# Optimization experiments

Hardware: AMD Instinct MI355X
Metric: run time of the kernel (lower is better)

The kernel has to match this reference:

```python
import jax, jax.numpy as jnp
import numpy as np

LEAKY = 0.2  # tf.nn.leaky_relu default alpha
E_SZ = [64, 64, 16]
F_SZ = [128, 128, 8]
N_MAPS, C, H, W = 64, 1, 32, 32
B = 8192


def _leaky(x):
    return jnp.where(x >= 0, x, LEAKY * x)


def func_theta(x, theta, sz, in_sz):
    # x: [B, in_sz]; theta: [B, total]; per-sample MLP with weights sliced from theta
    y = x
    offset = 0
    n = len(sz)
    for i, out_sz in enumerate(sz):
        w_sz = in_sz * out_sz
        Wm = theta[:, offset:offset + w_sz].reshape(-1, in_sz, out_sz)
        offset += w_sz
        b = theta[:, offset:offset + out_sz]
        offset += out_sz
        y = jnp.einsum('bi,bio->bo', y, Wm) + b
        if i < n - 1:
            y = _leaky(y)
        in_sz = out_sz
    return y


def setup_inputs() -> dict:
    key = jax.random.key(0)
    ks = jax.random.split(key, 16)

    def g(k, shape, scale):
        return (jax.random.normal(k, shape, dtype=jnp.float32) * scale)

    inp = {
        'indices': jax.random.randint(ks[0], (B,), 0, N_MAPS, dtype=jnp.int32),
        'states': jax.random.normal(ks[1], (B, 4), dtype=jnp.float32),
        'maps': jax.random.normal(ks[2], (N_MAPS, C, H, W), dtype=jnp.float32),
        'fc1_w': g(ks[3], (C * H * W, 256), 1.0 / np.sqrt(C * H * W)),
        'fc1_b': jnp.zeros((256,), jnp.float32),
        'fc2_w': g(ks[4], (256, 128), 1.0 / np.sqrt(256)),
        'fc2_b': jnp.zeros((128,), jnp.float32),
        'fc3_w': g(ks[5], (128, 128), 1.0 / np.sqrt(128)),
        'fc3_b': jnp.zeros((128,), jnp.float32),
        'bn_w': g(ks[6], (128, 32), 1.0 / np.sqrt(128)),
        'bn_b': jnp.zeros((32,), jnp.float32),
        'e_w': g(ks[7], (32, 5456), 1e-5),
        'e_b': g(ks[8], (5456,), 1e-3),
        'f_w': g(ks[9], (32, 21768), 1e-5),
        'f_b': g(ks[10], (21768,), 1e-3),
    }
    return inp


def reference(indices, states, maps, fc1_w, fc1_b, fc2_w, fc2_b, fc3_w, fc3_b,
              bn_w, bn_b, e_w, e_b, f_w, f_b):
    # gather maps per sample and flatten (NCHW -> NHWC transpose is a no-op after flatten
    # mathematically, but keep the exact data layout of the original)
    m = jnp.transpose(maps[indices], (0, 2, 3, 1)).astype(jnp.float32)  # [B,H,W,C]
    z = m.reshape(m.shape[0], -1)

    # hypernet trunk
    z = _leaky(z @ fc1_w + fc1_b)
    z = _leaky(z @ fc2_w + fc2_b)
    z = _leaky(z @ fc3_w + fc3_b)
    z = z @ bn_w + bn_b  # bottleneck, no activation
    theta_e = z @ e_w + e_b  # [B, 5456]
    theta_f = z @ f_w + f_b  # [B, 21768]

    S = states[:, 0:2]
    G = states[:, 2:4]
    e_s = func_theta(S, theta_e, E_SZ, 2)
    e_g = func_theta(G, theta_e, E_SZ, 2)
    zf = jnp.concatenate([e_s, e_g], axis=-1)  # [B, 32]
    ang = func_theta(zf, theta_f, F_SZ, 2 * E_SZ[-1])  # [B, 8]
    pts = jnp.concatenate([jnp.sin(ang), jnp.cos(ang)], axis=-1)  # [B, 16]
    return pts
```

## Files before the change

kernel.cpp:

```cpp
#include <hip/hip_runtime.h>
#include <hip/hip_bf16.h>


#define LEAKY 0.2f
#define NCLS 64
#define B_TOT 8192
#define CAP 48


__device__ __forceinline__ float lrelu(float x) { return x >= 0.f ? x : LEAKY * x; }

__global__ __launch_bounds__(1024) void fc1_kernel(
    const float* __restrict__ maps, const float* __restrict__ fc1_w,
    const float* __restrict__ fc1_b, float* __restrict__ h1g)
{
    __shared__ float m[1024];
    __shared__ float red[1024];
    const int t = threadIdx.x;
    const int c = blockIdx.x >> 2;
    const int q = blockIdx.x & 3;

    m[t] = maps[(size_t)c * 1024 + t];
    __syncthreads();

    const int ol = t & 63, ks = t >> 6;
    const int o = q * 64 + ol;
    const float* wp = fc1_w + o;
    float acc = 0.f;
#pragma unroll 8
    for (int i = 0; i < 64; ++i) {
        const int k = ks * 64 + i;
        acc += m[k] * wp[(size_t)k * 256];
    }
    red[t] = acc;
    __syncthreads();
    if (t < 64) {
        float a = fc1_b[q * 64 + t];
#pragma unroll
        for (int r = 0; r < 16; ++r) a += red[r * 64 + t];
        h1g[c * 256 + q * 64 + t] = lrelu(a);
    }
}

__global__ __launch_bounds__(1024) void backbone_bucket_kernel(
    const float* __restrict__ h1g,
    const float* __restrict__ fc2_w, const float* __restrict__ fc2_b,
    const float* __restrict__ fc3_w, const float* __restrict__ fc3_b,
    const float* __restrict__ bn_w,  const float* __restrict__ bn_b,
    float* __restrict__ z,
    const int* __restrict__ idx, int* __restrict__ counts,
    int* __restrict__ offsets, int* __restrict__ perm)
{
    __shared__ float red[1024];
    __shared__ float h1[256];
    __shared__ float h2[128];
    __shared__ float h3[128];
    __shared__ int cnt[16][64];
    __shared__ int wcur[16][64];

    const int t = threadIdx.x;

    if (blockIdx.x == 64) {
        const int w = t >> 6;
        cnt[w][t & 63] = 0;
        __syncthreads();
        int my[8];
#pragma unroll
        for (int r = 0; r < 8; ++r) {
            my[r] = idx[r * 1024 + t];
            atomicAdd(&cnt[w][my[r]], 1);
        }
        __syncthreads();
        if (t < 64) {
            int run = 0;
#pragma unroll
            for (int w2 = 0; w2 < 16; ++w2) {
                const int v = cnt[w2][t];
                wcur[w2][t] = run;
                run += v;
            }
            counts[t] = run;
            int x = run;
            for (int d = 1; d < 64; d <<= 1) {
                const int y = __shfl_up(x, d, 64);
                if (t >= d) x += y;
            }
            const int basec = x - run;
            offsets[t] = basec;
#pragma unroll
            for (int w2 = 0; w2 < 16; ++w2) wcur[w2][t] += basec;
        }
        __syncthreads();
#pragma unroll
        for (int r = 0; r < 8; ++r) {
            const int p = atomicAdd(&wcur[w][my[r]], 1);
            perm[p] = r * 1024 + t;
        }
        return;
    }

    const int c = blockIdx.x;
    if (t < 256) h1[t] = h1g[c * 256 + t];
    __syncthreads();

    {
        const int o = t & 127, ks = t >> 7;
        float acc = 0.f;
#pragma unroll
        for (int i = 0; i < 32; ++i) {
            const int k = ks * 32 + i;
            acc += h1[k] * fc2_w[k * 128 + o];
        }
        red[t] = acc;
    }
    __syncthreads();
    if (t < 128) {
        float a = fc2_b[t];
#pragma unroll
        for (int r = 0; r < 8; ++r) a += red[r * 128 + t];
        h2[t] = lrelu(a);
    }
    __syncthreads();
    {
        const int o = t & 127, ks = t >> 7;
        float acc = 0.f;
#pragma unroll
        for (int i = 0; i < 16; ++i) {
            const int k = ks * 16 + i;
            acc += h2[k] * fc3_w[k * 128 + o];
        }
        red[t] = acc;
    }
    __syncthreads();
    if (t < 128) {
        float a = fc3_b[t];
#pragma unroll
        for (int r = 0; r < 8; ++r) a += red[r * 128 + t];
        h3[t] = lrelu(a);
    }
    __syncthreads();
    {
        const int o = t & 31, ks = t >> 5;
        float acc = 0.f;
#pragma unroll
        for (int i = 0; i < 4; ++i) {
            const int k = ks * 4 + i;
            acc += h3[k] * bn_w[k * 32 + o];
        }
        red[t] = acc;
    }
    __syncthreads();
    if (t < 32) {
        float a = bn_b[t];
#pragma unroll
        for (int r = 0; r < 32; ++r) a += red[r * 32 + t];
        z[c * 32 + t] = a;
    }
}

__global__ __launch_bounds__(256) void theta_kernel(
    const float* __restrict__ z,
    const float* __restrict__ e_w, const float* __restrict__ e_b,
    const float* __restrict__ f_w, const float* __restrict__ f_b,
    float* __restrict__ th_e, float* __restrict__ th_f)
{
    __shared__ __align__(16) float zl[2048];
    const int t = threadIdx.x;
    ((float4*)zl)[t]       = ((const float4*)z)[t];
    ((float4*)zl)[t + 256] = ((const float4*)z)[t + 256];
    __syncthreads();

    int j = blockIdx.x * 256 + t;
    const int cbase = blockIdx.y * 8;
    const float* wbase;
    float* op;
    int stride;
    float bias;
    if (j < 5456) {
        wbase = e_w + j; bias = e_b[j]; op = th_e + j; stride = 5456;
    } else {
        const int jj = j - 5456;
        if (jj >= 21768) return;
        wbase = f_w + jj; bias = f_b[jj]; op = th_f + jj; stride = 21768;
    }
    float wk[32];
#pragma unroll
    for (int k = 0; k < 32; ++k) wk[k] = wbase[(size_t)k * stride];

#pragma unroll
    for (int cc = 0; cc < 8; cc += 4) {
        const int c0 = cbase + cc;
        float a0 = bias, a1 = bias, a2 = bias, a3 = bias;
#pragma unroll
        for (int k4 = 0; k4 < 8; ++k4) {
            const float4 z0 = *(const float4*)&zl[(c0 + 0) * 32 + k4 * 4];
            const float4 z1 = *(const float4*)&zl[(c0 + 1) * 32 + k4 * 4];
            const float4 z2 = *(const float4*)&zl[(c0 + 2) * 32 + k4 * 4];
            const float4 z3 = *(const float4*)&zl[(c0 + 3) * 32 + k4 * 4];
            const float w0 = wk[k4 * 4], w1 = wk[k4 * 4 + 1];
            const float w2 = wk[k4 * 4 + 2], w3 = wk[k4 * 4 + 3];
            a0 += z0.x * w0 + z0.y * w1 + z0.z * w2 + z0.w * w3;
            a1 += z1.x * w0 + z1.y * w1 + z1.z * w2 + z1.w * w3;
            a2 += z2.x * w0 + z2.y * w1 + z2.z * w2 + z2.w * w3;
            a3 += z3.x * w0 + z3.y * w1 + z3.z * w2 + z3.w * w3;
        }
        op[(size_t)(c0 + 0) * stride] = a0;
        op[(size_t)(c0 + 1) * stride] = a1;
        op[(size_t)(c0 + 2) * stride] = a2;
        op[(size_t)(c0 + 3) * stride] = a3;
    }
}

#define ESTRIDE 68
#define FSTRIDE 132

#define K3_LDS_FLOATS 32024
#define K3_LDS_BYTES  (K3_LDS_FLOATS * 4)

__global__ __launch_bounds__(512) void func_kernel(
    const float* __restrict__ states,
    const float* __restrict__ th_e_all, const float* __restrict__ th_f_all,
    const int* __restrict__ counts, const int* __restrict__ offsets,
    const int* __restrict__ perm, float* __restrict__ out)
{
    extern __shared__ float smem[];
    float* wE   = smem;
    float* wFa  = smem + 5392;
    float* wH   = smem + 10776;
    float* actA = smem + 18968;
    float* actB = smem + 25496;

    const int c = blockIdx.x;
    const int s = blockIdx.y;
    const int nb   = counts[c];
    const int base = offsets[c];
    const int q = nb >> 2, r = nb & 3;
    const int lo  = s * q + (s < r ? s : r);
    const int cnt = q + (s < r ? 1 : 0);
    if (cnt == 0) return;
    const int hi = lo + cnt;

    const float* te = th_e_all + (size_t)c * 5456;
    const float* tf = th_f_all + (size_t)c * 21768;

    const int t  = threadIdx.x;
    const int eg = t & 7,  vp = t >> 3;
    const int bp = t & 15, fg = t >> 4;
    const int cole = eg * 8;
    const int colf = fg * 8;
    const int col8 = t & 7, fb3 = t >> 3;

    for (int j = t * 4; j < 5392; j += 2048)
        *(float4*)&wE[j] = *(const float4*)&te[j];
    for (int j = t * 4; j < 4224; j += 2048)
        *(float4*)&wFa[j] = *(const float4*)&tf[j];
    for (int j = t * 4; j < 1160; j += 2048)
        *(float4*)&wFa[4224 + j] = *(const float4*)&tf[20608 + j];

    const int npass = (cnt + CAP - 1) / CAP;
    for (int p = 0; p < npass; ++p) {
        __syncthreads();

        for (int j = t * 4; j < 8192; j += 2048)
            *(float4*)&wH[j] = *(const float4*)&tf[4224 + j];

        const int pb = lo + p * CAP;

        if (t < 256) {
            const float4 wa0 = *(const float4*)&wE[cole];
            const float4 wa1 = *(const float4*)&wE[cole + 4];
            const float4 wb0 = *(const float4*)&wE[64 + cole];
            const float4 wb1 = *(const float4*)&wE[64 + cole + 4];
            const float4 bb0 = *(const float4*)&wE[128 + cole];
            const float4 bb1 = *(const float4*)&wE[128 + cole + 4];
#pragma unroll
            for (int sub = 0; sub < 3; ++sub) {
                const int vb = vp + 32 * sub;
                const int fb = vb >> 1, ve = vb & 1;
                const int ib = pb + fb;
                const int bi = (ib < hi) ? perm[base + ib] : 0;
                const float2 sv = *(const float2*)&states[(size_t)bi * 4 + 2 * ve];
                float4 o0, o1;
                o0.x = lrelu(sv.x * wa0.x + sv.y * wb0.x + bb0.x);
                o0.y = lrelu(sv.x * wa0.y + sv.y * wb0.y + bb0.y);
                o0.z = lrelu(sv.x * wa0.z + sv.y * wb0.z + bb0.z);
                o0.w = lrelu(sv.x * wa0.w + sv.y * wb0.w + bb0.w);
                o1.x = lrelu(sv.x * wa1.x + sv.y * wb1.x + bb1.x);
                o1.y = lrelu(sv.x * wa1.y + sv.y * wb1.y + bb1.y);
                o1.z = lrelu(sv.x * wa1.z + sv.y * wb1.z + bb1.z);
                o1.w = lrelu(sv.x * wa1.w + sv.y * wb1.w + bb1.w);
                *(float4*)&actA[vb * ESTRIDE + cole]     = o0;
                *(float4*)&actA[vb * ESTRIDE + cole + 4] = o1;
            }
        }
        __syncthreads();

        if (t < 256) {
            const int e0 = vp * ESTRIDE;
            const int e1 = (vp + 32) * ESTRIDE;
            const int e2 = (vp + 64) * ESTRIDE;
            float a0[8] = {0,0,0,0,0,0,0,0};
            float a1[8] = {0,0,0,0,0,0,0,0};
            float a2[8] = {0,0,0,0,0,0,0,0};
#pragma unroll 4
            for (int i4 = 0; i4 < 16; ++i4) {
                const float4 y0 = *(const float4*)&actA[e0 + i4 * 4];
                const float4 y1 = *(const float4*)&actA[e1 + i4 * 4];
                const float4 y2 = *(const float4*)&actA[e2 + i4 * 4];
#pragma unroll
                for (int u = 0; u < 4; ++u) {
                    const int row = 192 + (i4 * 4 + u) * 64 + cole;
                    const float4 wA = *(const float4*)&wE[row];
                    const float4 wB = *(const float4*)&wE[row + 4];
                    const float v0 = (&y0.x)[u], v1 = (&y1.x)[u], v2 = (&y2.x)[u];
                    a0[0] += v0 * wA.x; a0[1] += v0 * wA.y;
                    a0[2] += v0 * wA.z; a0[3] += v0 * wA.w;
                    a0[4] += v0 * wB.x; a0[5] += v0 * wB.y;
                    a0[6] += v0 * wB.z; a0[7] += v0 * wB.w;
                    a1[0] += v1 * wA.x; a1[1] += v1 * wA.y;
                    a1[2] += v1 * wA.z; a1[3] += v1 * wA.w;
                    a1[4] += v1 * wB.x; a1[5] += v1 * wB.y;
                    a1[6] += v1 * wB.z; a1[7] += v1 * wB.w;
                    a2[0] += v2 * wA.x; a2[1] += v2 * wA.y;
                    a2[2] += v2 * wA.z; a2[3] += v2 * wA.w;
                    a2[4] += v2 * wB.x; a2[5] += v2 * wB.y;
                    a2[6] += v2 * wB.z; a2[7] += v2 * wB.w;
                }
            }
            const float4 bA = *(const float4*)&wE[4288 + cole];
            const float4 bB = *(const float4*)&wE[4288 + cole + 4];
            float4 o0, o1;
            o0.x = lrelu(a0[0] + bA.x); o0.y = lrelu(a0[1] + bA.y);
            o0.z = lrelu(a0[2] + bA.z); o0.w = lrelu(a0[3] + bA.w);
            o1.x = lrelu(a0[4] + bB.x); o1.y = lrelu(a0[5] + bB.y);
            o1.z = lrelu(a0[6] + bB.z); o1.w = lrelu(a0[7] + bB.w);
            *(float4*)&actB[e0 + cole]     = o0;
            *(float4*)&actB[e0 + cole + 4] = o1;
            o0.x = lrelu(a1[0] + bA.x); o0.y = lrelu(a1[1] + bA.y);
            o0.z = lrelu(a1[2] + bA.z); o0.w = lrelu(a1[3] + bA.w);
            o1.x = lrelu(a1[4] + bB.x); o1.y = lrelu(a1[5] + bB.y);
            o1.z = lrelu(a1[6] + bB.z); o1.w = lrelu(a1[7] + bB.w);
            *(float4*)&actB[e1 + cole]     = o0;
            *(float4*)&actB[e1 + cole + 4] = o1;
            o0.x = lrelu(a2[0] + bA.x); o0.y = lrelu(a2[1] + bA.y);
            o0.z = lrelu(a2[2] + bA.z); o0.w = lrelu(a2[3] + bA.w);
            o1.x = lrelu(a2[4] + bB.x); o1.y = lrelu(a2[5] + bB.y);
            o1.z = lrelu(a2[6] + bB.z); o1.w = lrelu(a2[7] + bB.w);
            *(float4*)&actB[e2 + cole]     = o0;
            *(float4*)&actB[e2 + cole + 4] = o1;
        }
        __syncthreads();

        if (t < 256) {
            const int col3 = eg * 2;
            const int e0 = vp * ESTRIDE;
            const int e1 = (vp + 32) * ESTRIDE;
            const int e2 = (vp + 64) * ESTRIDE;
            float a00 = 0.f, a01 = 0.f, a10 = 0.f, a11 = 0.f, a20 = 0.f, a21 = 0.f;
#pragma unroll 4
            for (int i4 = 0; i4 < 16; ++i4) {
                const float4 y0 = *(const float4*)&actB[e0 + i4 * 4];
                const float4 y1 = *(const float4*)&actB[e1 + i4 * 4];
                const float4 y2 = *(const float4*)&actB[e2 + i4 * 4];
#pragma unroll
                for (int u = 0; u < 4; ++u) {
                    const float2 w2 = *(const float2*)&wE[4352 + (i4 * 4 + u) * 16 + col3];
                    const float v0 = (&y0.x)[u], v1 = (&y1.x)[u], v2 = (&y2.x)[u];
                    a00 += v0 * w2.x; a01 += v0 * w2.y;
                    a10 += v1 * w2.x; a11 += v1 * w2.y;
                    a20 += v2 * w2.x; a21 += v2 * w2.y;
                }
            }
            const float b0 = wE[5376 + col3], b1 = wE[5376 + col3 + 1];
            {
                const int vb = vp, fb = vb >> 1, ve = vb & 1;
                actA[fb * FSTRIDE + ve * 16 + col3]     = a00 + b0;
                actA[fb * FSTRIDE + ve * 16 + col3 + 1] = a01 + b1;
            }
            {
                const int vb = vp + 32, fb = vb >> 1, ve = vb & 1;
                actA[fb * FSTRIDE + ve * 16 + col3]     = a10 + b0;
                actA[fb * FSTRIDE + ve * 16 + col3 + 1] = a11 + b1;
            }
            {
                const int vb = vp + 64, fb = vb >> 1, ve = vb & 1;
                actA[fb * FSTRIDE + ve * 16 + col3]     = a20 + b0;
                actA[fb * FSTRIDE + ve * 16 + col3 + 1] = a21 + b1;
            }
        }
        __syncthreads();

        if (t < 256) {
            const int f0 = bp * FSTRIDE;
            const int f1 = (bp + 16) * FSTRIDE;
            const int f2 = (bp + 32) * FSTRIDE;
            float a0[8] = {0,0,0,0,0,0,0,0};
            float a1[8] = {0,0,0,0,0,0,0,0};
            float a2[8] = {0,0,0,0,0,0,0,0};
#pragma unroll
            for (int i4 = 0; i4 < 8; ++i4) {
                const float4 y0 = *(const float4*)&actA[f0 + i4 * 4];
                const float4 y1 = *(const float4*)&actA[f1 + i4 * 4];
                const float4 y2 = *(const float4*)&actA[f2 + i4 * 4];
#pragma unroll
                for (int u = 0; u < 4; ++u) {
                    const int row = (i4 * 4 + u) * 128 + colf;
                    const float4 wA = *(const float4*)&wFa[row];
                    const float4 wB = *(const float4*)&wFa[row + 4];
                    const float v0 = (&y0.x)[u], v1 = (&y1.x)[u], v2 = (&y2.x)[u];
                    a0[0] += v0 * wA.x; a0[1] += v0 * wA.y;
                    a0[2] += v0 * wA.z; a0[3] += v0 * wA.w;
                    a0[4] += v0 * wB.x; a0[5] += v0 * wB.y;
                    a0[6] += v0 * wB.z; a0[7] += v0 * wB.w;
                    a1[0] += v1 * wA.x; a1[1] += v1 * wA.y;
                    a1[2] += v1 * wA.z; a1[3] += v1 * wA.w;
                    a1[4] += v1 * wB.x; a1[5] += v1 * wB.y;
                    a1[6] += v1 * wB.z; a1[7] += v1 * wB.w;
                    a2[0] += v2 * wA.x; a2[1] += v2 * wA.y;
                    a2[2] += v2 * wA.z; a2[3] += v2 * wA.w;
                    a2[4] += v2 * wB.x; a2[5] += v2 * wB.y;
                    a2[6] += v2 * wB.z; a2[7] += v2 * wB.w;
                }
            }
            const float4 bA = *(const float4*)&wFa[4096 + colf];
            const float4 bB = *(const float4*)&wFa[4096 + colf + 4];
            float4 o0, o1;
            o0.x = lrelu(a0[0] + bA.x); o0.y = lrelu(a0[1] + bA.y);
            o0.z = lrelu(a0[2] + bA.z); o0.w = lrelu(a0[3] + bA.w);
            o1.x = lrelu(a0[4] + bB.x); o1.y = lrelu(a0[5] + bB.y);
            o1.z = lrelu(a0[6] + bB.z); o1.w = lrelu(a0[7] + bB.w);
            *(float4*)&actB[f0 + colf]     = o0;
            *(float4*)&actB[f0 + colf + 4] = o1;
            o0.x = lrelu(a1[0] + bA.x); o0.y = lrelu(a1[1] + bA.y);
            o0.z = lrelu(a1[2] + bA.z); o0.w = lrelu(a1[3] + bA.w);
            o1.x = lrelu(a1[4] + bB.x); o1.y = lrelu(a1[5] + bB.y);
            o1.z = lrelu(a1[6] + bB.z); o1.w = lrelu(a1[7] + bB.w);
            *(float4*)&actB[f1 + colf]     = o0;
            *(float4*)&actB[f1 + colf + 4] = o1;
            o0.x = lrelu(a2[0] + bA.x); o0.y = lrelu(a2[1] + bA.y);
            o0.z = lrelu(a2[2] + bA.z); o0.w = lrelu(a2[3] + bA.w);
            o1.x = lrelu(a2[4] + bB.x); o1.y = lrelu(a2[5] + bB.y);
            o1.z = lrelu(a2[6] + bB.z); o1.w = lrelu(a2[7] + bB.w);
            *(float4*)&actB[f2 + colf]     = o0;
            *(float4*)&actB[f2 + colf + 4] = o1;
        }
        __syncthreads();

        {
            const int f0 = bp * FSTRIDE;
            const int f1 = (bp + 16) * FSTRIDE;
            const int f2 = (bp + 32) * FSTRIDE;
            float a0[8] = {0,0,0,0,0,0,0,0};
            float a1[8] = {0,0,0,0,0,0,0,0};
            float a2[8] = {0,0,0,0,0,0,0,0};
            if (t < 256) {
#pragma unroll 4
                for (int i4 = 0; i4 < 16; ++i4) {
                    const float4 y0 = *(const float4*)&actB[f0 + i4 * 4];
                    const float4 y1 = *(const float4*)&actB[f1 + i4 * 4];
                    const float4 y2 = *(const float4*)&actB[f2 + i4 * 4];
#pragma unroll
                    for (int u = 0; u < 4; ++u) {
                        const int row = (i4 * 4 + u) * 128 + colf;
                        const float4 wA = *(const float4*)&wH[row];
                        const float4 wB = *(const float4*)&wH[row + 4];
                        const float v0 = (&y0.x)[u], v1 = (&y1.x)[u], v2 = (&y2.x)[u];
                        a0[0] += v0 * wA.x; a0[1] += v0 * wA.y;
                        a0[2] += v0 * wA.z; a0[3] += v0 * wA.w;
                        a0[4] += v0 * wB.x; a0[5] += v0 * wB.y;
                        a0[6] += v0 * wB.z; a0[7] += v0 * wB.w;
                        a1[0] += v1 * wA.x; a1[1] += v1 * wA.y;
                        a1[2] += v1 * wA.z; a1[3] += v1 * wA.w;
                        a1[4] += v1 * wB.x; a1[5] += v1 * wB.y;
                        a1[6] += v1 * wB.z; a1[7] += v1 * wB.w;
                        a2[0] += v2 * wA.x; a2[1] += v2 * wA.y;
                        a2[2] += v2 * wA.z; a2[3] += v2 * wA.w;
                        a2[4] += v2 * wB.x; a2[5] += v2 * wB.y;
                        a2[6] += v2 * wB.z; a2[7] += v2 * wB.w;
                    }
                }
            }
            __syncthreads();
            for (int j = t * 4; j < 8192; j += 2048)
                *(float4*)&wH[j] = *(const float4*)&tf[4224 + 8192 + j];
            __syncthreads();
            if (t < 256) {
#pragma unroll 4
                for (int i4 = 0; i4 < 16; ++i4) {
                    const float4 y0 = *(const float4*)&actB[f0 + 64 + i4 * 4];
                    const float4 y1 = *(const float4*)&actB[f1 + 64 + i4 * 4];
                    const float4 y2 = *(const float4*)&actB[f2 + 64 + i4 * 4];
#pragma unroll
                    for (int u = 0; u < 4; ++u) {
                        const int row = (i4 * 4 + u) * 128 + colf;
                        const float4 wA = *(const float4*)&wH[row];
                        const float4 wB = *(const float4*)&wH[row + 4];
                        const float v0 = (&y0.x)[u], v1 = (&y1.x)[u], v2 = (&y2.x)[u];
                        a0[0] += v0 * wA.x; a0[1] += v0 * wA.y;
                        a0[2] += v0 * wA.z; a0[3] += v0 * wA.w;
                        a0[4] += v0 * wB.x; a0[5] += v0 * wB.y;
                        a0[6] += v0 * wB.z; a0[7] += v0 * wB.w;
                        a1[0] += v1 * wA.x; a1[1] += v1 * wA.y;
                        a1[2] += v1 * wA.z; a1[3] += v1 * wA.w;
                        a1[4] += v1 * wB.x; a1[5] += v1 * wB.y;
                        a1[6] += v1 * wB.z; a1[7] += v1 * wB.w;
                        a2[0] += v2 * wA.x; a2[1] += v2 * wA.y;
                        a2[2] += v2 * wA.z; a2[3] += v2 * wA.w;
                        a2[4] += v2 * wB.x; a2[5] += v2 * wB.y;
                        a2[6] += v2 * wB.z; a2[7] += v2 * wB.w;
                    }
                }
                const float4 bA = *(const float4*)&wFa[4224 + colf];
                const float4 bB = *(const float4*)&wFa[4224 + colf + 4];
                float4 o0, o1;
                o0.x = lrelu(a0[0] + bA.x); o0.y = lrelu(a0[1] + bA.y);
                o0.z = lrelu(a0[2] + bA.z); o0.w = lrelu(a0[3] + bA.w);
                o1.x = lrelu(a0[4] + bB.x); o1.y = lrelu(a0[5] + bB.y);
                o1.z = lrelu(a0[6] + bB.z); o1.w = lrelu(a0[7] + bB.w);
                *(float4*)&actA[f0 + colf]     = o0;
                *(float4*)&actA[f0 + colf + 4] = o1;
                o0.x = lrelu(a1[0] + bA.x); o0.y = lrelu(a1[1] + bA.y);
                o0.z = lrelu(a1[2] + bA.z); o0.w = lrelu(a1[3] + bA.w);
                o1.x = lrelu(a1[4] + bB.x); o1.y = lrelu(a1[5] + bB.y);
                o1.z = lrelu(a1[6] + bB.z); o1.w = lrelu(a1[7] + bB.w);
                *(float4*)&actA[f1 + colf]     = o0;
                *(float4*)&actA[f1 + colf + 4] = o1;
                o0.x = lrelu(a2[0] + bA.x); o0.y = lrelu(a2[1] + bA.y);
                o0.z = lrelu(a2[2] + bA.z); o0.w = lrelu(a2[3] + bA.w);
                o1.x = lrelu(a2[4] + bB.x); o1.y = lrelu(a2[5] + bB.y);
                o1.z = lrelu(a2[6] + bB.z); o1.w = lrelu(a2[7] + bB.w);
                *(float4*)&actA[f2 + colf]     = o0;
                *(float4*)&actA[f2 + colf + 4] = o1;
            }
        }
        __syncthreads();

        if (fb3 < CAP) {
            const int ib = pb + fb3;
            if (ib < hi) {
                const int foff = fb3 * FSTRIDE;
                float a = 0.f;
#pragma unroll 8
                for (int i4 = 0; i4 < 32; ++i4) {
                    const float4 y4 = *(const float4*)&actA[foff + i4 * 4];
#pragma unroll
                    for (int u = 0; u < 4; ++u)
                        a += (&y4.x)[u] * wFa[4352 + (i4 * 4 + u) * 8 + col8];
                }
                a += wFa[5376 + col8];
                const int bi = perm[base + ib];
                out[(size_t)bi * 16 + col8]     = __sinf(a);
                out[(size_t)bi * 16 + 8 + col8] = __cosf(a);
            }
        }
    }
}

extern "C" void kernel_launch(void* const* d_in, const int* in_sizes, int n_in,
                              void* d_out, int out_size, void* d_ws, size_t ws_size,
                              hipStream_t stream)
{
    const int*   indices = (const int*)  d_in[0];
    const float* states  = (const float*)d_in[1];
    const float* maps    = (const float*)d_in[2];
    const float* fc1_w   = (const float*)d_in[3];
    const float* fc1_b   = (const float*)d_in[4];
    const float* fc2_w   = (const float*)d_in[5];
    const float* fc2_b   = (const float*)d_in[6];
    const float* fc3_w   = (const float*)d_in[7];
    const float* fc3_b   = (const float*)d_in[8];
    const float* bn_w    = (const float*)d_in[9];
    const float* bn_b    = (const float*)d_in[10];
    const float* e_w     = (const float*)d_in[11];
    const float* e_b     = (const float*)d_in[12];
    const float* f_w     = (const float*)d_in[13];
    const float* f_b     = (const float*)d_in[14];
    float* out = (float*)d_out;

    float* ws   = (float*)d_ws;
    float* z    = ws;
    float* th_e = ws + 2048;
    float* th_f = ws + 351232;
    int* counts  = (int*)(ws + 1744384);
    int* offsets = counts + 64;
    int* perm    = counts + 128;
    float* h1g   = ws + 1752704;

    static int s_lds_optin = 0;
    if (!s_lds_optin) {
        hipFuncSetAttribute((const void*)func_kernel,
                            hipFuncAttributeMaxDynamicSharedMemorySize,
                            K3_LDS_BYTES);
        s_lds_optin = 1;
    }

    fc1_kernel<<<256, 1024, 0, stream>>>(maps, fc1_w, fc1_b, h1g);
    backbone_bucket_kernel<<<65, 1024, 0, stream>>>(
        h1g, fc2_w, fc2_b, fc3_w, fc3_b, bn_w, bn_b, z,
        indices, counts, offsets, perm);
    theta_kernel<<<dim3(107, 8), 256, 0, stream>>>(
        z, e_w, e_b, f_w, f_b, th_e, th_f);
    func_kernel<<<dim3(NCLS, 4), 512, K3_LDS_BYTES, stream>>>(
        states, th_e, th_f, counts, offsets, perm, out);
}
```

Baseline: 130.5 us.

## Keep both F-layer-2 weight halves resident in LDS and transpose F3 weights

Loads both 64-row halves of the 128x128 F hidden weight into separate LDS buffers once per block, instead of reloading them from global memory every pass with two extra barriers. To fit the larger LDS footprint, CAP drops from 48 to 44 samples per pass, and the third row-group is guarded so that padding rows are neither computed into outputs nor stored. The final 128x8 weight is stored transposed with padding, so each thread reads float4 vectors instead of strided scalars. The cost is more LDS per block, which may lower occupancy, plus more passes for large groups.

Measured after the change: 149.6 us. +14.7%, slower.

```diff
diff --git a/kernel.cpp b/kernel.cpp
--- a/kernel.cpp
+++ b/kernel.cpp
@@ -5,7 +5,7 @@
 #define LEAKY 0.2f
 #define NCLS 64
 #define B_TOT 8192
-#define CAP 48
+#define CAP 44
 
 
 __device__ __forceinline__ float lrelu(float x) { return x >= 0.f ? x : LEAKY * x; }
@@ -214,7 +214,11 @@
 #define ESTRIDE 68
 #define FSTRIDE 132
 
-#define K3_LDS_FLOATS 32024
+#define WFA_B2F  4224
+#define WFA_B3F  4352
+#define WFA_W3T  4360
+
+#define K3_LDS_FLOATS 39160
 #define K3_LDS_BYTES  (K3_LDS_FLOATS * 4)
 
 __global__ __launch_bounds__(512) void func_kernel(
@@ -226,9 +230,10 @@
     extern __shared__ float smem[];
     float* wE   = smem;
     float* wFa  = smem + 5392;
-    float* wH   = smem + 10776;
-    float* actA = smem + 18968;
-    float* actB = smem + 25496;
+    float* wH   = smem + 10808;
+    float* wH2  = smem + 19000;
+    float* actA = smem + 27192;
+    float* actB = smem + 33176;
 
     const int c = blockIdx.x;
     const int s = blockIdx.y;
@@ -249,20 +254,25 @@
     const int cole = eg * 8;
     const int colf = fg * 8;
     const int col8 = t & 7, fb3 = t >> 3;
+    const bool e_has2 = (vp < 24);
+    const bool f_has2 = (bp < 12);
 
     for (int j = t * 4; j < 5392; j += 2048)
         *(float4*)&wE[j] = *(const float4*)&te[j];
     for (int j = t * 4; j < 4224; j += 2048)
         *(float4*)&wFa[j] = *(const float4*)&tf[j];
-    for (int j = t * 4; j < 1160; j += 2048)
-        *(float4*)&wFa[4224 + j] = *(const float4*)&tf[20608 + j];
+    if (t < 128) wFa[WFA_B2F + t] = tf[20608 + t];
+    if (t < 8)   wFa[WFA_B3F + t] = tf[21760 + t];
+    for (int j = t; j < 1024; j += 512)
+        wFa[WFA_W3T + (j & 7) * 132 + (j >> 3)] = tf[20736 + j];
+    for (int j = t * 4; j < 8192; j += 2048)
+        *(float4*)&wH[j]  = *(const float4*)&tf[4224 + j];
+    for (int j = t * 4; j < 8192; j += 2048)
+        *(float4*)&wH2[j] = *(const float4*)&tf[12416 + j];
 
     const int npass = (cnt + CAP - 1) / CAP;
     for (int p = 0; p < npass; ++p) {
         __syncthreads();
-
-        for (int j = t * 4; j < 8192; j += 2048)
-            *(float4*)&wH[j] = *(const float4*)&tf[4224 + j];
 
         const int pb = lo + p * CAP;
 
@@ -276,6 +286,7 @@
 #pragma unroll
             for (int sub = 0; sub < 3; ++sub) {
                 const int vb = vp + 32 * sub;
+                if (vb >= 88) break;
                 const int fb = vb >> 1, ve = vb & 1;
                 const int ib = pb + fb;
                 const int bi = (ib < hi) ? perm[base + ib] : 0;
@@ -298,7 +309,7 @@
         if (t < 256) {
             const int e0 = vp * ESTRIDE;
             const int e1 = (vp + 32) * ESTRIDE;
-            const int e2 = (vp + 64) * ESTRIDE;
+            const int e2 = e_has2 ? (vp + 64) * ESTRIDE : e0;
             float a0[8] = {0,0,0,0,0,0,0,0};
             float a1[8] = {0,0,0,0,0,0,0,0};
             float a2[8] = {0,0,0,0,0,0,0,0};
@@ -342,12 +353,14 @@
             o1.z = lrelu(a1[6] + bB.z); o1.w = lrelu(a1[7] + bB.w);
             *(float4*)&actB[e1 + cole]     = o0;
             *(float4*)&actB[e1 + cole + 4] = o1;
-            o0.x = lrelu(a2[0] + bA.x); o0.y = lrelu(a2[1] + bA.y);
-            o0.z = lrelu(a2[2] + bA.z); o0.w = lrelu(a2[3] + bA.w);
-            o1.x = lrelu(a2[4] + bB.x); o1.y = lrelu(a2[5] + bB.y);
-            o1.z = lrelu(a2[6] + bB.z); o1.w = lrelu(a2[7] + bB.w);
-            *(float4*)&actB[e2 + cole]     = o0;
-            *(float4*)&actB[e2 + cole + 4] = o1;
+            if (e_has2) {
+                o0.x = lrelu(a2[0] + bA.x); o0.y = lrelu(a2[1] + bA.y);
+                o0.z = lrelu(a2[2] + bA.z); o0.w = lrelu(a2[3] + bA.w);
+                o1.x = lrelu(a2[4] + bB.x); o1.y = lrelu(a2[5] + bB.y);
+                o1.z = lrelu(a2[6] + bB.z); o1.w = lrelu(a2[7] + bB.w);
+                *(float4*)&actB[e2 + cole]     = o0;
+                *(float4*)&actB[e2 + cole + 4] = o1;
+            }
         }
         __syncthreads();
 
@@ -355,7 +368,7 @@
             const int col3 = eg * 2;
             const int e0 = vp * ESTRIDE;
             const int e1 = (vp + 32) * ESTRIDE;
-            const int e2 = (vp + 64) * ESTRIDE;
+            const int e2 = e_has2 ? (vp + 64) * ESTRIDE : e0;
             float a00 = 0.f, a01 = 0.f, a10 = 0.f, a11 = 0.f, a20 = 0.f, a21 = 0.f;
 #pragma unroll 4
             for (int i4 = 0; i4 < 16; ++i4) {
@@ -382,7 +395,7 @@
                 actA[fb * FSTRIDE + ve * 16 + col3]     = a10 + b0;
                 actA[fb * FSTRIDE + ve * 16 + col3 + 1] = a11 + b1;
             }
-            {
+            if (e_has2) {
                 const int vb = vp + 64, fb = vb >> 1, ve = vb & 1;
                 actA[fb * FSTRIDE + ve * 16 + col3]     = a20 + b0;
                 actA[fb * FSTRIDE + ve * 16 + col3 + 1] = a21 + b1;
@@ -393,7 +406,7 @@
         if (t < 256) {
             const int f0 = bp * FSTRIDE;
             const int f1 = (bp + 16) * FSTRIDE;
-            const int f2 = (bp + 32) * FSTRIDE;
+            const int f2 = f_has2 ? (bp + 32) * FSTRIDE : f0;
             float a0[8] = {0,0,0,0,0,0,0,0};
             float a1[8] = {0,0,0,0,0,0,0,0};
             float a2[8] = {0,0,0,0,0,0,0,0};
@@ -437,94 +450,90 @@
             o1.z = lrelu(a1[6] + bB.z); o1.w = lrelu(a1[7] + bB.w);
             *(float4*)&actB[f1 + colf]     = o0;
             *(float4*)&actB[f1 + colf + 4] = o1;
-            o0.x = lrelu(a2[0] + bA.x); o0.y = lrelu(a2[1] + bA.y);
-            o0.z = lrelu(a2[2] + bA.z); o0.w = lrelu(a2[3] + bA.w);
-            o1.x = lrelu(a2[4] + bB.x); o1.y = lrelu(a2[5] + bB.y);
-            o1.z = lrelu(a2[6] + bB.z); o1.w = lrelu(a2[7] + bB.w);
-            *(float4*)&actB[f2 + colf]     = o0;
-            *(float4*)&actB[f2 + colf + 4] = o1;
-        }
-        __syncthreads();
-
-        {
+            if (f_has2) {
+                o0.x = lrelu(a2[0] + bA.x); o0.y = lrelu(a2[1] + bA.y);
+                o0.z = lrelu(a2[2] + bA.z); o0.w = lrelu(a2[3] + bA.w);
+                o1.x = lrelu(a2[4] + bB.x); o1.y = lrelu(a2[5] + bB.y);
+                o1.z = lrelu(a2[6] + bB.z); o1.w = lrelu(a2[7] + bB.w);
+                *(float4*)&actB[f2 + colf]     = o0;
+                *(float4*)&actB[f2 + colf + 4] = o1;
+            }
+        }
+        __syncthreads();
+
+        if (t < 256) {
             const int f0 = bp * FSTRIDE;
             const int f1 = (bp + 16) * FSTRIDE;
-            const int f2 = (bp + 32) * FSTRIDE;
+            const int f2 = f_has2 ? (bp + 32) * FSTRIDE : f0;
             float a0[8] = {0,0,0,0,0,0,0,0};
             float a1[8] = {0,0,0,0,0,0,0,0};
             float a2[8] = {0,0,0,0,0,0,0,0};
-            if (t < 256) {
 #pragma unroll 4
-                for (int i4 = 0; i4 < 16; ++i4) {
-                    const float4 y0 = *(const float4*)&actB[f0 + i4 * 4];
-                    const float4 y1 = *(const float4*)&actB[f1 + i4 * 4];
-                    const float4 y2 = *(const float4*)&actB[f2 + i4 * 4];
-#pragma unroll
-                    for (int u = 0; u < 4; ++u) {
-                        const int row = (i4 * 4 + u) * 128 + colf;
-                        const float4 wA = *(const float4*)&wH[row];
-                        const float4 wB = *(const float4*)&wH[row + 4];
-                        const float v0 = (&y0.x)[u], v1 = (&y1.x)[u], v2 = (&y2.x)[u];
-                        a0[0] += v0 * wA.x; a0[1] += v0 * wA.y;
-                        a0[2] += v0 * wA.z; a0[3] += v0 * wA.w;
-                        a0[4] += v0 * wB.x; a0[5] += v0 * wB.y;
-                        a0[6] += v0 * wB.z; a0[7] += v0 * wB.w;
-                        a1[0] += v1 * wA.x; a1[1] += v1 * wA.y;
-                        a1[2] += v1 * wA.z; a1[3] += v1 * wA.w;
-                        a1[4] += v1 * wB.x; a1[5] += v1 * wB.y;
-                        a1[6] += v1 * wB.z; a1[7] += v1 * wB.w;
-                        a2[0] += v2 * wA.x; a2[1] += v2 * wA.y;
-                        a2[2] += v2 * wA.z; a2[3] += v2 * wA.w;
-                        a2[4] += v2 * wB.x; a2[5] += v2 * wB.y;
-                        a2[6] += v2 * wB.z; a2[7] += v2 * wB.w;
-                    }
+            for (int i4 = 0; i4 < 16; ++i4) {
+                const float4 y0 = *(const float4*)&actB[f0 + i4 * 4];
+                const float4 y1 = *(const float4*)&actB[f1 + i4 * 4];
+                const float4 y2 = *(const float4*)&actB[f2 + i4 * 4];
+#pragma unroll
+                for (int u = 0; u < 4; ++u) {
+                    const int row = (i4 * 4 + u) * 128 + colf;
+                    const float4 wA = *(const float4*)&wH[row];
+                    const float4 wB = *(const float4*)&wH[row + 4];
+                    const float v0 = (&y0.x)[u], v1 = (&y1.x)[u], v2 = (&y2.x)[u];
+                    a0[0] += v0 * wA.x; a0[1] += v0 * wA.y;
+                    a0[2] += v0 * wA.z; a0[3] += v0 * wA.w;
+                    a0[4] += v0 * wB.x; a0[5] += v0 * wB.y;
+                    a0[6] += v0 * wB.z; a0[7] += v0 * wB.w;
+                    a1[0] += v1 * wA.x; a1[1] += v1 * wA.y;
+                    a1[2] += v1 * wA.z; a1[3] += v1 * wA.w;
+                    a1[4] += v1 * wB.x; a1[5] += v1 * wB.y;
+                    a1[6] += v1 * wB.z; a1[7] += v1 * wB.w;
+                    a2[0] += v2 * wA.x; a2[1] += v2 * wA.y;
+                    a2[2] += v2 * wA.z; a2[3] += v2 * wA.w;
+                    a2[4] += v2 * wB.x; a2[5] += v2 * wB.y;
+                    a2[6] += v2 * wB.z; a2[7] += v2 * wB.w;
                 }
             }
-            __syncthreads();
-            for (int j = t * 4; j < 8192; j += 2048)
-                *(float4*)&wH[j] = *(const float4*)&tf[4224 + 8192 + j];
-            __syncthreads();
-            if (t < 256) {
 #pragma unroll 4
-                for (int i4 = 0; i4 < 16; ++i4) {
-                    const float4 y0 = *(const float4*)&actB[f0 + 64 + i4 * 4];
-                    const float4 y1 = *(const float4*)&actB[f1 + 64 + i4 * 4];
-                    const float4 y2 = *(const float4*)&actB[f2 + 64 + i4 * 4];
-#pragma unroll
-                    for (int u = 0; u < 4; ++u) {
-                        const int row = (i4 * 4 + u) * 128 + colf;
-                        const float4 wA = *(const float4*)&wH[row];
-                        const float4 wB = *(const float4*)&wH[row + 4];
-                        const float v0 = (&y0.x)[u], v1 = (&y1.x)[u], v2 = (&y2.x)[u];
-                        a0[0] += v0 * wA.x; a0[1] += v0 * wA.y;
-                        a0[2] += v0 * wA.z; a0[3] += v0 * wA.w;
-                        a0[4] += v0 * wB.x; a0[5] += v0 * wB.y;
-                        a0[6] += v0 * wB.z; a0[7] += v0 * wB.w;
-                        a1[0] += v1 * wA.x; a1[1] += v1 * wA.y;
-                        a1[2] += v1 * wA.z; a1[3] += v1 * wA.w;
-                        a1[4] += v1 * wB.x; a1[5] += v1 * wB.y;
-                        a1[6] += v1 * wB.z; a1[7] += v1 * wB.w;
-                        a2[0] += v2 * wA.x; a2[1] += v2 * wA.y;
-                        a2[2] += v2 * wA.z; a2[3] += v2 * wA.w;
-                        a2[4] += v2 * wB.x; a2[5] += v2 * wB.y;
-                        a2[6] += v2 * wB.z; a2[7] += v2 * wB.w;
-                    }
+            for (int i4 = 0; i4 < 16; ++i4) {
+                const float4 y0 = *(const float4*)&actB[f0 + 64 + i4 * 4];
+                const float4 y1 = *(const float4*)&actB[f1 + 64 + i4 * 4];
+                const float4 y2 = *(const float4*)&actB[f2 + 64 + i4 * 4];
+#pragma unroll
+                for (int u = 0; u < 4; ++u) {
+                    const int row = (i4 * 4 + u) * 128 + colf;
+                    const float4 wA = *(const float4*)&wH2[row];
+                    const float4 wB = *(const float4*)&wH2[row + 4];
+                    const float v0 = (&y0.x)[u], v1 = (&y1.x)[u], v2 = (&y2.x)[u];
+                    a0[0] += v0 * wA.x; a0[1] += v0 * wA.y;
+                    a0[2] += v0 * wA.z; a0[3] += v0 * wA.w;
+                    a0[4] += v0 * wB.x; a0[5] += v0 * wB.y;
+                    a0[6] += v0 * wB.z; a0[7] += v0 * wB.w;
+                    a1[0] += v1 * wA.x; a1[1] += v1 * wA.y;
+                    a1[2] += v1 * wA.z; a1[3] += v1 * wA.w;
+                    a1[4] += v1 * wB.x; a1[5] += v1 * wB.y;
+                    a1[6] += v1 * wB.z; a1[7] += v1 * wB.w;
+                    a2[0] += v2 * wA.x; a2[1] += v2 * wA.y;
+                    a2[2] += v2 * wA.z; a2[3] += v2 * wA.w;
+                    a2[4] += v2 * wB.x; a2[5] += v2 * wB.y;
+                    a2[6] += v2 * wB.z; a2[7] += v2 * wB.w;
                 }
-                const float4 bA = *(const float4*)&wFa[4224 + colf];
-                const float4 bB = *(const float4*)&wFa[4224 + colf + 4];
-                float4 o0, o1;
-                o0.x = lrelu(a0[0] + bA.x); o0.y = lrelu(a0[1] + bA.y);
-                o0.z = lrelu(a0[2] + bA.z); o0.w = lrelu(a0[3] + bA.w);
-                o1.x = lrelu(a0[4] + bB.x); o1.y = lrelu(a0[5] + bB.y);
-                o1.z = lrelu(a0[6] + bB.z); o1.w = lrelu(a0[7] + bB.w);
-                *(float4*)&actA[f0 + colf]     = o0;
-                *(float4*)&actA[f0 + colf + 4] = o1;
-                o0.x = lrelu(a1[0] + bA.x); o0.y = lrelu(a1[1] + bA.y);
-                o0.z = lrelu(a1[2] + bA.z); o0.w = lrelu(a1[3] + bA.w);
-                o1.x = lrelu(a1[4] + bB.x); o1.y = lrelu(a1[5] + bB.y);
-                o1.z = lrelu(a1[6] + bB.z); o1.w = lrelu(a1[7] + bB.w);
-                *(float4*)&actA[f1 + colf]     = o0;
-                *(float4*)&actA[f1 + colf + 4] = o1;
+            }
+            const float4 bA = *(const float4*)&wFa[WFA_B2F + colf];
+            const float4 bB = *(const float4*)&wFa[WFA_B2F + colf + 4];
+            float4 o0, o1;
+            o0.x = lrelu(a0[0] + bA.x); o0.y = lrelu(a0[1] + bA.y);
+            o0.z = lrelu(a0[2] + bA.z); o0.w = lrelu(a0[3] + bA.w);
+            o1.x = lrelu(a0[4] + bB.x); o1.y = lrelu(a0[5] + bB.y);
+            o1.z = lrelu(a0[6] + bB.z); o1.w = lrelu(a0[7] + bB.w);
+            *(float4*)&actA[f0 + colf]     = o0;
+            *(float4*)&actA[f0 + colf + 4] = o1;
+            o0.x = lrelu(a1[0] + bA.x); o0.y = lrelu(a1[1] + bA.y);
+            o0.z = lrelu(a1[2] + bA.z); o0.w = lrelu(a1[3] + bA.w);
+            o1.x = lrelu(a1[4] + bB.x); o1.y = lrelu(a1[5] + bB.y);
+            o1.z = lrelu(a1[6] + bB.z); o1.w = lrelu(a1[7] + bB.w);
+            *(float4*)&actA[f1 + colf]     = o0;
+            *(float4*)&actA[f1 + colf + 4] = o1;
+            if (f_has2) {
                 o0.x = lrelu(a2[0] + bA.x); o0.y = lrelu(a2[1] + bA.y);
                 o0.z = lrelu(a2[2] + bA.z); o0.w = lrelu(a2[3] + bA.w);
                 o1.x = lrelu(a2[4] + bB.x); o1.y = lrelu(a2[5] + bB.y);
@@ -539,15 +548,15 @@
             const int ib = pb + fb3;
             if (ib < hi) {
                 const int foff = fb3 * FSTRIDE;
+                const int wb = WFA_W3T + col8 * 132;
                 float a = 0.f;
 #pragma unroll 8
                 for (int i4 = 0; i4 < 32; ++i4) {
                     const float4 y4 = *(const float4*)&actA[foff + i4 * 4];
-#pragma unroll
-                    for (int u = 0; u < 4; ++u)
-                        a += (&y4.x)[u] * wFa[4352 + (i4 * 4 + u) * 8 + col8];
+                    const float4 w4 = *(const float4*)&wFa[wb + i4 * 4];
+                    a += y4.x * w4.x + y4.y * w4.y + y4.z * w4.z + y4.w * w4.w;
                 }
-                a += wFa[5376 + col8];
+                a += wFa[WFA_B3F + col8];
                 const int bi = perm[base + ib];
                 out[(size_t)bi * 16 + col8]     = __sinf(a);
                 out[(size_t)bi * 16 + 8 + col8] = __cosf(a);
```
